# Kernel tuning notes

Hardware: AMD Instinct MI355X
Metric: run time of the kernel (lower is better)

## Reference

```python
import jax, jax.numpy as jnp
import numpy as np

T, B, C, H, W = 4, 8, 256, 16, 16
HEADS = 8
N = H * W
TN = T * N
DH = C // HEADS
DECAY = 0.25

# STE quantizer: fwd round(clamp(x,0,1)); bwd passes grad only where 0<=x<=1
@jax.custom_vjp
def quant1(x):
    return jnp.round(jnp.clip(x, 0.0, 1.0))

def _q_fwd(x):
    return quant1(x), x

def _q_bwd(x, g):
    return (jnp.where((x < 0) | (x > 1), 0.0, g),)

quant1.defvjp(_q_fwd, _q_bwd)

def lif(x):
    # x: [T, ...]; sequential LIF membrane decay + quantize over leading (time) axis
    def step(carry, xt):
        mem_old, spike = carry
        mem = (mem_old - jax.lax.stop_gradient(spike) * 0.5) * DECAY + xt
        s = quant1(mem)
        return (mem, s), s
    z = jnp.zeros_like(x[0])
    _, out = jax.lax.scan(step, (z, z), x)
    return out

def bn1d(x, gamma, beta, mean, var):
    # eval-mode BatchNorm1d over channel axis 1 of [B, Ch, L]
    inv = jax.lax.rsqrt(var + 1e-5)
    return (x - mean[None, :, None]) * (gamma * inv)[None, :, None] + beta[None, :, None]

def _rel_pos_index():
    coords = np.stack(np.meshgrid(np.arange(T), np.arange(H), np.arange(W), indexing='ij'))  # [3,T,H,W]
    cf = coords.reshape(3, -1)                      # [3, TN]
    rc = (cf[:, :, None] - cf[:, None, :]).transpose(1, 2, 0).copy()  # [TN, TN, 3]
    rc[:, :, 0] += T - 1
    rc[:, :, 1] += H - 1
    rc[:, :, 2] += W - 1
    rc[:, :, 0] *= (2 * H - 1) * (2 * W - 1)
    rc[:, :, 1] *= (2 * W - 1)
    return rc.sum(-1)                               # [TN, TN] ints

def _mask():
    m = np.ones((TN, TN), np.float32)
    for t in range(T - 1):
        m[t * N:(t + 1) * N, (t + 1) * N:] = 0.0
    return m

_RPI = jnp.asarray(_rel_pos_index().reshape(-1))
_MASK = jnp.asarray(_mask())


def setup_inputs() -> dict:
    key = jax.random.key(0)
    ks = jax.random.split(key, 13)
    bias_rows = (2 * T - 1) * (2 * H - 1) * (2 * W - 1)
    return {
        'x': jax.random.normal(ks[0], (T, B, C, H, W), jnp.float32),
        'w_qkv': jax.random.normal(ks[1], (3 * C, C), jnp.float32) * 0.05,
        'qkv_gamma': jax.random.uniform(ks[2], (3 * C,), jnp.float32, 0.5, 1.5),
        'qkv_beta': jax.random.normal(ks[3], (3 * C,), jnp.float32) * 0.1,
        'qkv_mean': jax.random.normal(ks[4], (3 * C,), jnp.float32) * 0.1,
        'qkv_var': jax.random.uniform(ks[5], (3 * C,), jnp.float32, 0.5, 1.5),
        'bias_table': jax.random.normal(ks[6], (bias_rows, HEADS), jnp.float32) * 0.02,
        'w_proj': jax.random.normal(ks[7], (C, C), jnp.float32) * 0.05,
        'b_proj': jax.random.normal(ks[8], (C,), jnp.float32) * 0.02,
        'proj_gamma': jax.random.uniform(ks[9], (C,), jnp.float32, 0.5, 1.5),
        'proj_beta': jax.random.normal(ks[10], (C,), jnp.float32) * 0.1,
        'proj_mean': jax.random.normal(ks[11], (C,), jnp.float32) * 0.1,
        'proj_var': jax.random.uniform(ks[12], (C,), jnp.float32, 0.5, 1.5),
    }


def reference(x, w_qkv, qkv_gamma, qkv_beta, qkv_mean, qkv_var, bias_table,
              w_proj, b_proj, proj_gamma, proj_beta, proj_mean, proj_var):
    # flatten spatial, then raw reshape [T,B,C,N] -> [B,C,T*N] (as in torch source)
    xf = x.reshape(T, B, C, N).reshape(B, C, T * N)
    # 1x1 conv == channel matmul, then eval BN
    qkv = jnp.einsum('oc,bcl->bol', w_qkv, xf)
    qkv = bn1d(qkv, qkv_gamma, qkv_beta, qkv_mean, qkv_var)
    qkv = qkv.reshape(B, 3 * C, T, N).transpose(2, 0, 1, 3)  # [T,B,3C,N]
    qkv = lif(qkv).transpose(1, 0, 3, 2)                      # [B,T,N,3C]
    q, k, v = jnp.split(qkv, 3, axis=-1)                      # each [B,T,N,C]

    def to_heads(z):  # b t n (h d) -> b h (t n) d
        return z.reshape(B, T, N, HEADS, DH).transpose(0, 3, 1, 2, 4).reshape(B, HEADS, TN, DH)
    q, k, v = map(to_heads, (q, k, v))

    bias = bias_table[_RPI].reshape(TN, TN, HEADS).transpose(2, 0, 1)  # [h,TN,TN]
    attn = jnp.einsum('bhnd,bhmd->bhnm', q, k) + bias[None]
    attn = attn * _MASK[None, None]                                     # block upper-triangle mask
    o = jnp.einsum('bhnm,bhmd->bhnd', attn, v) * 0.125                  # [B,h,TN,d]

    o = o.transpose(0, 2, 1, 3).reshape(B, TN, C).reshape(B, T, N, C).transpose(1, 0, 3, 2)  # [T,B,C,N]
    o = lif(o)
    o = o.transpose(1, 2, 0, 3).reshape(B, C, T * N)          # [B,C,TN]
    o = jnp.einsum('oc,bcl->bol', w_proj, o) + b_proj[None, :, None]
    o = bn1d(o, proj_gamma, proj_beta, proj_mean, proj_var)
    o = o.reshape(B, C, T, N).transpose(2, 0, 1, 3).reshape(T, B, C, H, W)
    return lif(o)
```

## Files before the change

### kernel.cpp

```cpp
#include <hip/hip_runtime.h>
#include <stdint.h>
#include <math.h>

constexpr int T_ = 4;
constexpr int B_ = 8;
constexpr int C_ = 256;
constexpr int N_ = 256;
constexpr int TN_ = 1024;
constexpr int NH_ = 8;
constexpr int O3_ = 768;
constexpr int BIAS_ROWS_ = 6727;

__device__ __constant__ int TI_OF[10] = {0,1,1,2,2,2,3,3,3,3};
__device__ __constant__ int TJ_OF[10] = {0,0,1,0,1,2,0,1,2,3};

__device__ __forceinline__ float quant1f(float m) {
    return rintf(fminf(fmaxf(m, 0.0f), 1.0f));
}

__global__ __launch_bounds__(256) void k1_qkv_gemm(
    const float* __restrict__ x, const float* __restrict__ w,
    const float* __restrict__ gamma, const float* __restrict__ beta,
    const float* __restrict__ mean, const float* __restrict__ var,
    float* __restrict__ out)
{
    __shared__ float At[32][36];
    __shared__ float Bt[32][132];
    const int b = blockIdx.z;
    const int oBase = blockIdx.y * 32;
    const int lBase = blockIdx.x * 128;
    const int tid = threadIdx.x;
    const int tx = tid & 31;
    const int ty = tid >> 5;
    const float* xb = x + (size_t)b * C_ * TN_;

    float acc[4][4];
#pragma unroll
    for (int i = 0; i < 4; ++i)
#pragma unroll
        for (int j = 0; j < 4; ++j) acc[i][j] = 0.0f;

    const int a_row0 = tid >> 4, a_k2 = (tid & 15) * 2;
    const int b_kk0 = tid >> 5, b_c4 = (tid & 31) * 4;

    for (int kc = 0; kc < 8; ++kc) {
        const int k0 = kc * 32;
#pragma unroll
        for (int r = 0; r < 2; ++r) {
            const int row = a_row0 + 16 * r;
            const float2 v = *(const float2*)&w[(size_t)(oBase + row) * C_ + k0 + a_k2];
            At[a_k2][row] = v.x;
            At[a_k2 + 1][row] = v.y;
        }
#pragma unroll
        for (int r = 0; r < 4; ++r) {
            const int kk = b_kk0 + 8 * r;
            const float4 v = *(const float4*)&xb[(size_t)(k0 + kk) * TN_ + lBase + b_c4];
            *(float4*)&Bt[kk][b_c4] = v;
        }
        __syncthreads();
#pragma unroll
        for (int cc = 0; cc < 32; ++cc) {
            float a[4], bb[4];
            *(float4*)&a[0] = *(const float4*)&At[cc][ty * 4];
            *(float4*)&bb[0] = *(const float4*)&Bt[cc][tx * 4];
#pragma unroll
            for (int i = 0; i < 4; ++i)
#pragma unroll
                for (int j = 0; j < 4; ++j) acc[i][j] += a[i] * bb[j];
        }
        __syncthreads();
    }

#pragma unroll
    for (int i = 0; i < 4; ++i) {
        const int o = oBase + ty * 4 + i;
        const float inv = 1.0f / sqrtf(var[o] + 1e-5f);
        const float g = gamma[o] * inv;
        const float mn = mean[o], bt = beta[o];
        float4 st;
        st.x = (acc[i][0] - mn) * g + bt;
        st.y = (acc[i][1] - mn) * g + bt;
        st.z = (acc[i][2] - mn) * g + bt;
        st.w = (acc[i][3] - mn) * g + bt;
        *(float4*)&out[((size_t)b * O3_ + o) * TN_ + lBase + tx * 4] = st;
    }
}

__global__ __launch_bounds__(256) void k2_lif_pack(
    const float* __restrict__ qkv,
    uint32_t* __restrict__ qb, uint32_t* __restrict__ kb, uint32_t* __restrict__ vb)
{
    const int n = threadIdx.x;
    const int g = blockIdx.x;
    const int b = blockIdx.y;
    const int dq = blockIdx.z;
    const int which = g >> 3, h = g & 7;
    uint32_t* dstw = (which == 0) ? qb : (which == 1) ? kb : vb;
    uint8_t* dst = (uint8_t*)dstw;
    const float* src = qkv + ((size_t)b * O3_ + g * 32 + dq * 8) * TN_;

    float memv[8];
#pragma unroll
    for (int d = 0; d < 8; ++d) memv[d] = 0.0f;
    uint32_t prev = 0;

    for (int t = 0; t < T_; ++t) {
        uint32_t bits = 0;
#pragma unroll
        for (int d = 0; d < 8; ++d) {
            const float xv = src[(size_t)d * TN_ + t * N_ + n];
            const float m = (memv[d] - 0.5f * (float)((prev >> d) & 1u)) * 0.25f + xv;
            memv[d] = m;
            const float s = quant1f(m);
            bits |= ((uint32_t)s) << d;
        }
        prev = bits;
        dst[4 * (((size_t)b * NH_ + h) * TN_ + t * N_ + n) + dq] = (uint8_t)bits;
    }
}

__global__ __launch_bounds__(256) void k3_tgp(
    const uint32_t* __restrict__ kb, const uint32_t* __restrict__ vb,
    int* __restrict__ Pt)
{
    __shared__ uint64_t ks[32][4];
    __shared__ uint64_t vs[32][4];
    const int t = blockIdx.x;
    const int bh = blockIdx.y;
    const int tid = threadIdx.x;
    const int q = tid >> 6, lane = tid & 63;
    const int j = t * N_ + q * 64 + lane;

    const uint32_t kw = kb[(size_t)bh * TN_ + j];
    const uint32_t vw = vb[(size_t)bh * TN_ + j];
#pragma unroll
    for (int d = 0; d < 32; ++d) {
        const uint64_t mk = __ballot((kw >> d) & 1u);
        const uint64_t mv = __ballot((vw >> d) & 1u);
        if (lane == 0) { ks[d][q] = mk; vs[d][q] = mv; }
    }
    __syncthreads();

    const int d = tid & 31;
#pragma unroll
    for (int s = 0; s < 4; ++s) {
        const int d2 = (tid >> 5) + 8 * s;
        int p = 0;
#pragma unroll
        for (int w = 0; w < 4; ++w) p += __popcll(ks[d2][w] & vs[d][w]);
        Pt[(size_t)(bh * 4 + t) * 1024 + d2 * 32 + d] = p;
    }
}

__global__ __launch_bounds__(256) void k3_cum(
    const int* __restrict__ Pt, float* __restrict__ Gf)
{
    const int bh = blockIdx.x;
    const int tid = threadIdx.x;
#pragma unroll
    for (int r = 0; r < 4; ++r) {
        const int idx = tid + 256 * r;
        int cum = 0;
#pragma unroll
        for (int t = 0; t < T_; ++t) {
            cum += Pt[(size_t)(bh * 4 + t) * 1024 + idx];
            Gf[(size_t)(bh * 4 + t) * 1024 + idx] = (float)cum;
        }
    }
}

__global__ __launch_bounds__(256) void k3_bias_gemm(
    const uint32_t* __restrict__ vb, const float* __restrict__ bias_table,
    float* __restrict__ p0, float* __restrict__ p1,
    float* __restrict__ p2, float* __restrict__ p3)
{
    __shared__ float sbl[544];
    __shared__ float At[32][36];
    __shared__ float Bt[32][132];

    const int z = blockIdx.z;
    const int h = z / 10;
    const int p = z % 10;
    const int ti = TI_OF[p], tj = TJ_OF[p];
    const int dt = ti - tj;
    const int iT = blockIdx.y;
    const int nBase = blockIdx.x * 128;
    const int tid = threadIdx.x;

    const int base = 3363 + 961 * dt + 62 * iT - 480;
    for (int s = tid; s < 544; s += 256) {
        const int gidx = base + s;
        sbl[s] = (gidx >= 0 && gidx < BIAS_ROWS_) ? bias_table[(size_t)gidx * NH_ + h] : 0.0f;
    }

    const int ty2 = tid >> 4, tx16 = tid & 15;

    const int il0 = ty2 * 2;
    const int sRowBase = 480 + 31 * (il0 >> 4) + (il0 & 15) - tx16;

    const int n8 = tx16 * 8;
    const int nS = nBase + n8;
    const int bS = nS >> 5, d0S = nS & 31;
    const uint32_t* vbw = vb + ((size_t)bS * NH_ + h) * TN_ + tj * 256 + ty2;

    const int tyc = tid >> 5, txc = tid & 31;
    const int nA = nBase + txc * 4;
    const int bA = nA >> 5, dA = nA & 31;

    float acc[4][4];
#pragma unroll
    for (int i = 0; i < 4; ++i)
#pragma unroll
        for (int j = 0; j < 4; ++j) acc[i][j] = 0.0f;

    __syncthreads();

    for (int kc = 0; kc < 8; ++kc) {
#pragma unroll
        for (int r1 = 0; r1 < 2; ++r1) {
            const int s0 = sRowBase - 31 * (kc * 2 + r1);
            float2 av;
            av.x = sbl[s0];
            av.y = sbl[s0 + 1];
            At[tx16 + 16 * r1][il0] = av.x;
            At[tx16 + 16 * r1][il0 + 1] = av.y;
        }
#pragma unroll
        for (int r = 0; r < 2; ++r) {
            const uint32_t wd = vbw[kc * 32 + 16 * r];
            float4 b0, b1;
            b0.x = (float)((wd >> d0S) & 1u);
            b0.y = (float)((wd >> (d0S + 1)) & 1u);
            b0.z = (float)((wd >> (d0S + 2)) & 1u);
            b0.w = (float)((wd >> (d0S + 3)) & 1u);
            b1.x = (float)((wd >> (d0S + 4)) & 1u);
            b1.y = (float)((wd >> (d0S + 5)) & 1u);
            b1.z = (float)((wd >> (d0S + 6)) & 1u);
            b1.w = (float)((wd >> (d0S + 7)) & 1u);
            *(float4*)&Bt[ty2 + 16 * r][n8] = b0;
            *(float4*)&Bt[ty2 + 16 * r][n8 + 4] = b1;
        }
        __syncthreads();
#pragma unroll
        for (int cc = 0; cc < 32; ++cc) {
            float a[4], bb[4];
            *(float4*)&a[0] = *(const float4*)&At[cc][tyc * 4];
            *(float4*)&bb[0] = *(const float4*)&Bt[cc][txc * 4];
#pragma unroll
            for (int i = 0; i < 4; ++i)
#pragma unroll
                for (int j = 0; j < 4; ++j) acc[i][j] += a[i] * bb[j];
        }
        __syncthreads();
    }

    float* plane = (tj == 0) ? p0 : (tj == 1) ? p1 : (tj == 2) ? p2 : p3;
    const int nrows = (4 - tj) * 256;
    const int cA = h * 32 + dA;
#pragma unroll
    for (int r = 0; r < 4; ++r) {
        const int rowL = dt * 256 + iT * 32 + tyc * 4 + r;
        float4 s0;
        s0.x = acc[r][0]; s0.y = acc[r][1]; s0.z = acc[r][2]; s0.w = acc[r][3];
        *(float4*)&plane[((size_t)bA * nrows + rowL) * 256 + cA] = s0;
    }
}

__global__ __launch_bounds__(256) void k4_lif2(
    const uint32_t* __restrict__ qb, const float* __restrict__ Gf,
    const float* __restrict__ p0, const float* __restrict__ p1,
    const float* __restrict__ p2, const float* __restrict__ p3,
    uint32_t* __restrict__ s2c)
{
    const int c = threadIdx.x;
    const int n = blockIdx.x;
    const int b = blockIdx.y;
    const int lane = c & 63;
    const int h = c >> 5, d = c & 31;
    const int bh = b * NH_ + h;
    const uint32_t* qbh = qb + (size_t)bh * TN_;

    float memv = 0.0f, spk = 0.0f;
    for (int t = 0; t < T_; ++t) {
        const int l = t * N_ + n;
        const uint32_t q = qbh[l];
        const float* g = Gf + (size_t)(bh * 4 + t) * 1024 + d;
        float v = 0.0f;
#pragma unroll
        for (int d2 = 0; d2 < 32; ++d2)
            v += ((q >> d2) & 1u) ? g[d2 * 32] : 0.0f;
        v += p0[((size_t)b * 1024 + l) * 256 + c];
        if (t >= 1) v += p1[((size_t)b * 768 + (l - 256)) * 256 + c];
        if (t >= 2) v += p2[((size_t)b * 512 + (l - 512)) * 256 + c];
        if (t >= 3) v += p3[((size_t)b * 256 + (l - 768)) * 256 + c];
        const float m = (memv - 0.5f * spk) * 0.25f + 0.125f * v;
        memv = m;
        const float s = quant1f(m);
        spk = s;
        const uint64_t mask = __ballot(s != 0.0f);
        if (lane == 0)
            s2c[((size_t)b * TN_ + l) * 8 + (c >> 5)] = (uint32_t)mask;
        else if (lane == 32)
            s2c[((size_t)b * TN_ + l) * 8 + (c >> 5)] = (uint32_t)(mask >> 32);
    }
}

__global__ __launch_bounds__(256) void k5_proj_lif(
    const uint32_t* __restrict__ s2c, const float* __restrict__ w,
    const float* __restrict__ bp,
    const float* __restrict__ gamma, const float* __restrict__ beta,
    const float* __restrict__ mean, const float* __restrict__ var,
    float* __restrict__ out)
{
    __shared__ float At[128][36];
    __shared__ uint32_t Sw[128 * 9];
    const int nBase = blockIdx.x * 32;
    const int oBase = blockIdx.y * 32;
    const int b = blockIdx.z;
    const int tid = threadIdx.x;
    const int tx = tid & 31;
    const int ty = tid >> 5;

#pragma unroll
    for (int j = 0; j < 4; ++j) {
        const int fidx = tid * 4 + j;
        const int lp = fidx >> 3, wsel = fidx & 7;
        const int t = lp >> 5, nn = lp & 31;
        Sw[lp * 9 + wsel] = s2c[((size_t)b * TN_ + t * 256 + nBase + nn) * 8 + wsel];
    }

    const int a_row = tid >> 3, a_kq = (tid & 7) * 16;

    float acc[4][4];
#pragma unroll
    for (int r = 0; r < 4; ++r)
#pragma unroll
        for (int t = 0; t < 4; ++t) acc[r][t] = 0.0f;

    for (int half = 0; half < 2; ++half) {
        if (half) __syncthreads();
#pragma unroll
        for (int j = 0; j < 4; ++j) {
            const float4 v = *(const float4*)&w[(size_t)(oBase + a_row) * C_ + half * 128 + a_kq + 4 * j];
            At[a_kq + 4 * j][a_row] = v.x;
            At[a_kq + 4 * j + 1][a_row] = v.y;
            At[a_kq + 4 * j + 2][a_row] = v.z;
            At[a_kq + 4 * j + 3][a_row] = v.w;
        }
        __syncthreads();

        for (int ks = 0; ks < 4; ++ks) {
            uint32_t wr[4];
#pragma unroll
            for (int t = 0; t < 4; ++t)
                wr[t] = Sw[(t * 32 + tx) * 9 + half * 4 + ks];
#pragma unroll
            for (int u = 0; u < 32; ++u) {
                float a[4];
                *(float4*)&a[0] = *(const float4*)&At[ks * 32 + u][ty * 4];
                float bv[4];
#pragma unroll
                for (int t = 0; t < 4; ++t) bv[t] = (float)((wr[t] >> u) & 1u);
#pragma unroll
                for (int r = 0; r < 4; ++r)
#pragma unroll
                    for (int t = 0; t < 4; ++t) acc[r][t] += a[r] * bv[t];
            }
        }
    }

#pragma unroll
    for (int r = 0; r < 4; ++r) {
        const int o = oBase + ty * 4 + r;
        const float inv = 1.0f / sqrtf(var[o] + 1e-5f);
        const float g = gamma[o] * inv;
        const float mn = mean[o], bt = beta[o], bpo = bp[o];
        float memv = 0.0f, spk = 0.0f;
#pragma unroll
        for (int t = 0; t < 4; ++t) {
            const float val = ((acc[r][t] + bpo) - mn) * g + bt;
            const float m = (memv - 0.5f * spk) * 0.25f + val;
            memv = m;
            const float s = quant1f(m);
            spk = s;
            out[(((size_t)t * B_ + b) * C_ + o) * N_ + nBase + tx] = s;
        }
    }
}

extern "C" void kernel_launch(void* const* d_in, const int* in_sizes, int n_in,
                              void* d_out, int out_size, void* d_ws, size_t ws_size,
                              hipStream_t stream)
{
    const float* x          = (const float*)d_in[0];
    const float* w_qkv      = (const float*)d_in[1];
    const float* qkv_gamma  = (const float*)d_in[2];
    const float* qkv_beta   = (const float*)d_in[3];
    const float* qkv_mean   = (const float*)d_in[4];
    const float* qkv_var    = (const float*)d_in[5];
    const float* bias_table = (const float*)d_in[6];
    const float* w_proj     = (const float*)d_in[7];
    const float* b_proj     = (const float*)d_in[8];
    const float* proj_gamma = (const float*)d_in[9];
    const float* proj_beta  = (const float*)d_in[10];
    const float* proj_mean  = (const float*)d_in[11];
    const float* proj_var   = (const float*)d_in[12];
    float* out = (float*)d_out;

    char* ws = (char*)d_ws;
    float*    qkv_bn = (float*)(ws + 0);
    float*    part0  = (float*)(ws + 1048576);
    float*    part1  = (float*)(ws + 9437184);
    float*    part2  = (float*)(ws + 15728640);
    float*    part3  = (float*)(ws + 19922944);
    float*    Gf     = (float*)(ws + 25165824);
    int*      Pt     = (int*)  (ws + 26214400);
    uint32_t* s2c    = (uint32_t*)(ws + 33554432);
    uint32_t* qbits  = (uint32_t*)(ws + 50331648);
    uint32_t* kbits  = (uint32_t*)(ws + 50593792);
    uint32_t* vbits  = (uint32_t*)(ws + 50855936);

    k1_qkv_gemm<<<dim3(8, 24, 8), 256, 0, stream>>>(
        x, w_qkv, qkv_gamma, qkv_beta, qkv_mean, qkv_var, qkv_bn);

    k2_lif_pack<<<dim3(24, 8, 4), 256, 0, stream>>>(qkv_bn, qbits, kbits, vbits);

    k3_tgp<<<dim3(4, 64), 256, 0, stream>>>(kbits, vbits, Pt);

    k3_cum<<<dim3(64), 256, 0, stream>>>(Pt, Gf);

    k3_bias_gemm<<<dim3(2, 8, 80), 256, 0, stream>>>(
        vbits, bias_table, part0, part1, part2, part3);

    k4_lif2<<<dim3(256, 8), 256, 0, stream>>>(
        qbits, Gf, part0, part1, part2, part3, s2c);

    k5_proj_lif<<<dim3(8, 8, 8), 256, 0, stream>>>(
        s2c, w_proj, b_proj, proj_gamma, proj_beta, proj_mean, proj_var, out);
}
```

Baseline: 220.9 us.

## Enlarge QKV GEMM tile to 64x128 and prefetch next K-slice into registers

The QKV projection GEMM tile grows from 32 to 64 output rows per block, giving each thread an 8x4 accumulator and halving the grid in the output dimension. Global loads for the next K chunk are issued into registers before the current chunk's compute, then written to shared memory after a barrier. This software pipelining hides global load latency and improves arithmetic intensity per block. The cost is higher register pressure and fewer blocks (768), which may lower occupancy. Only the first of several kernels changes.

```diff
diff --git a/kernel.cpp b/kernel.cpp
--- a/kernel.cpp
+++ b/kernel.cpp
@@ -24,57 +24,87 @@
     const float* __restrict__ mean, const float* __restrict__ var,
     float* __restrict__ out)
 {
-    __shared__ float At[32][36];
+    __shared__ float At[32][68];
     __shared__ float Bt[32][132];
     const int b = blockIdx.z;
-    const int oBase = blockIdx.y * 32;
+    const int oBase = blockIdx.y * 64;
     const int lBase = blockIdx.x * 128;
     const int tid = threadIdx.x;
-    const int tx = tid & 31;
-    const int ty = tid >> 5;
     const float* xb = x + (size_t)b * C_ * TN_;
 
-    float acc[4][4];
-#pragma unroll
-    for (int i = 0; i < 4; ++i)
+    const int tyc = tid >> 5;
+    const int txc = tid & 31;
+
+    const int a_row0 = tid >> 4;
+    const int a_k2 = (tid & 15) * 2;
+    const int b_k0 = tid >> 5;
+    const int b_n4 = (tid & 31) * 4;
+
+    float acc[8][4];
+#pragma unroll
+    for (int i = 0; i < 8; ++i)
 #pragma unroll
         for (int j = 0; j < 4; ++j) acc[i][j] = 0.0f;
 
-    const int a_row0 = tid >> 4, a_k2 = (tid & 15) * 2;
-    const int b_kk0 = tid >> 5, b_c4 = (tid & 31) * 4;
+    float2 aR[4];
+    float4 bR[4];
+
+#pragma unroll
+    for (int r = 0; r < 4; ++r)
+        aR[r] = *(const float2*)&w[(size_t)(oBase + a_row0 + 16 * r) * C_ + a_k2];
+#pragma unroll
+    for (int r = 0; r < 4; ++r)
+        bR[r] = *(const float4*)&xb[(size_t)(b_k0 + 8 * r) * TN_ + lBase + b_n4];
+#pragma unroll
+    for (int r = 0; r < 4; ++r) {
+        const int row = a_row0 + 16 * r;
+        At[a_k2][row] = aR[r].x;
+        At[a_k2 + 1][row] = aR[r].y;
+    }
+#pragma unroll
+    for (int r = 0; r < 4; ++r)
+        *(float4*)&Bt[b_k0 + 8 * r][b_n4] = bR[r];
+    __syncthreads();
 
     for (int kc = 0; kc < 8; ++kc) {
-        const int k0 = kc * 32;
-#pragma unroll
-        for (int r = 0; r < 2; ++r) {
-            const int row = a_row0 + 16 * r;
-            const float2 v = *(const float2*)&w[(size_t)(oBase + row) * C_ + k0 + a_k2];
-            At[a_k2][row] = v.x;
-            At[a_k2 + 1][row] = v.y;
-        }
-#pragma unroll
-        for (int r = 0; r < 4; ++r) {
-            const int kk = b_kk0 + 8 * r;
-            const float4 v = *(const float4*)&xb[(size_t)(k0 + kk) * TN_ + lBase + b_c4];
-            *(float4*)&Bt[kk][b_c4] = v;
+        if (kc < 7) {
+            const int k0 = (kc + 1) * 32;
+#pragma unroll
+            for (int r = 0; r < 4; ++r)
+                aR[r] = *(const float2*)&w[(size_t)(oBase + a_row0 + 16 * r) * C_ + k0 + a_k2];
+#pragma unroll
+            for (int r = 0; r < 4; ++r)
+                bR[r] = *(const float4*)&xb[(size_t)(k0 + b_k0 + 8 * r) * TN_ + lBase + b_n4];
+        }
+#pragma unroll
+        for (int cc = 0; cc < 32; ++cc) {
+            float a[8], bb[4];
+            *(float4*)&a[0] = *(const float4*)&At[cc][tyc * 8];
+            *(float4*)&a[4] = *(const float4*)&At[cc][tyc * 8 + 4];
+            *(float4*)&bb[0] = *(const float4*)&Bt[cc][txc * 4];
+#pragma unroll
+            for (int i = 0; i < 8; ++i)
+#pragma unroll
+                for (int j = 0; j < 4; ++j) acc[i][j] += a[i] * bb[j];
         }
         __syncthreads();
-#pragma unroll
-        for (int cc = 0; cc < 32; ++cc) {
-            float a[4], bb[4];
-            *(float4*)&a[0] = *(const float4*)&At[cc][ty * 4];
-            *(float4*)&bb[0] = *(const float4*)&Bt[cc][tx * 4];
-#pragma unroll
-            for (int i = 0; i < 4; ++i)
-#pragma unroll
-                for (int j = 0; j < 4; ++j) acc[i][j] += a[i] * bb[j];
-        }
-        __syncthreads();
-    }
-
-#pragma unroll
-    for (int i = 0; i < 4; ++i) {
-        const int o = oBase + ty * 4 + i;
+        if (kc < 7) {
+#pragma unroll
+            for (int r = 0; r < 4; ++r) {
+                const int row = a_row0 + 16 * r;
+                At[a_k2][row] = aR[r].x;
+                At[a_k2 + 1][row] = aR[r].y;
+            }
+#pragma unroll
+            for (int r = 0; r < 4; ++r)
+                *(float4*)&Bt[b_k0 + 8 * r][b_n4] = bR[r];
+            __syncthreads();
+        }
+    }
+
+#pragma unroll
+    for (int i = 0; i < 8; ++i) {
+        const int o = oBase + tyc * 8 + i;
         const float inv = 1.0f / sqrtf(var[o] + 1e-5f);
         const float g = gamma[o] * inv;
         const float mn = mean[o], bt = beta[o];
@@ -83,7 +113,7 @@
         st.y = (acc[i][1] - mn) * g + bt;
         st.z = (acc[i][2] - mn) * g + bt;
         st.w = (acc[i][3] - mn) * g + bt;
-        *(float4*)&out[((size_t)b * O3_ + o) * TN_ + lBase + tx * 4] = st;
+        *(float4*)&out[((size_t)b * O3_ + o) * TN_ + lBase + txc * 4] = st;
     }
 }
 
@@ -421,7 +451,7 @@
     uint32_t* kbits  = (uint32_t*)(ws + 50593792);
     uint32_t* vbits  = (uint32_t*)(ws + 50855936);
 
-    k1_qkv_gemm<<<dim3(8, 24, 8), 256, 0, stream>>>(
+    k1_qkv_gemm<<<dim3(8, 12, 8), 256, 0, stream>>>(
         x, w_qkv, qkv_gamma, qkv_beta, qkv_mean, qkv_var, qkv_bn);
 
     k2_lif_pack<<<dim3(24, 8, 4), 256, 0, stream>>>(qkv_bn, qbits, kbits, vbits);
```

After: 250.5 us. 1.13x slower.
